# Kernel optimization log

Hardware: AMD Instinct MI355X
Metric: run time of the kernel (lower is better)

The kernel has to match this reference:

```python
import jax, jax.numpy as jnp
import numpy as np

EPS = 1e-5

def _layernorm(x, gamma, beta):
    mu = jnp.mean(x, axis=-1, keepdims=True)
    var = jnp.mean(jnp.square(x - mu), axis=-1, keepdims=True)
    return (x - mu) * jax.lax.rsqrt(var + EPS) * gamma + beta

def setup_inputs() -> dict:
    key = jax.random.key(0)
    k_in, k_w, k_b = jax.random.split(key, 3)
    d_model, d_proj, n_tok = 1024, 256, 65536
    inputs = jax.random.normal(k_in, (n_tok, d_model), dtype=jnp.float32)
    # LayerNorm(d_model) params (torch default init: gamma=1, beta=0)
    ln1_g = jnp.ones((d_model,), jnp.float32)
    ln1_b = jnp.zeros((d_model,), jnp.float32)
    # Linear(d_model, d_proj): torch stores weight as [d_proj, d_model]
    bound = 1.0 / np.sqrt(d_model)
    W = jax.random.uniform(k_w, (d_proj, d_model), jnp.float32, -bound, bound)
    b = jax.random.uniform(k_b, (d_proj,), jnp.float32, -bound, bound)
    ln2_g = jnp.ones((d_proj,), jnp.float32)
    ln2_b = jnp.zeros((d_proj,), jnp.float32)
    return {"inputs": inputs, "ln1_g": ln1_g, "ln1_b": ln1_b, "W": W, "b": b,
            "ln2_g": ln2_g, "ln2_b": ln2_b}

def reference(inputs, ln1_g, ln1_b, W, b, ln2_g, ln2_b):
    h = _layernorm(inputs, ln1_g, ln1_b)          # [N, d_model]
    h = jnp.einsum('nd,pd->np', h, W) + b          # [N, d_proj]
    return _layernorm(h, ln2_g, ln2_b)             # [N, d_proj]
```

## Files before the change

kernel.cpp:

```cpp
#include <hip/hip_runtime.h>
#include <stdint.h>


#define D_MODEL 1024
#define D_PROJ  256
#define BM      64
#define BK      32
#define KITERS  32
#define NTHR    512
#define XSTR    40
#define EPS     1e-5f

typedef __attribute__((ext_vector_type(4))) float  f32x4;
typedef __attribute__((ext_vector_type(8))) __bf16 bf16x8;

__device__ __forceinline__ void gll16(const void* g, void* l) {
  __builtin_amdgcn_global_load_lds(
      (const __attribute__((address_space(1))) uint32_t*)g,
      (__attribute__((address_space(3))) uint32_t*)l, 16, 0, 0);
}

__global__ __launch_bounds__(256) void prep_kernel(
    const float* __restrict__ W, const float* __restrict__ g1,
    const float* __restrict__ b1, const float* __restrict__ bias,
    __bf16* __restrict__ wh, __bf16* __restrict__ wl,
    float* __restrict__ s1, float* __restrict__ s2) {
  const int p = blockIdx.x;
  const int t = threadIdx.x;
  f32x4 w4  = *(const f32x4*)(W  + (size_t)p * D_MODEL + t * 4);
  f32x4 g4  = *(const f32x4*)(g1 + t * 4);
  f32x4 b14 = *(const f32x4*)(b1 + t * 4);
  union { __bf16 h[4]; uint64_t u; } ph, pl;
  float a = 0.f, c = 0.f;
#pragma unroll
  for (int j = 0; j < 4; ++j) {
    float wg = w4[j] * g4[j];
    a += wg;
    c += b14[j] * w4[j];
    __bf16 hb = (__bf16)wg;
    ph.h[j] = hb;
    pl.h[j] = (__bf16)(wg - (float)hb);
  }
  const int cc = t >> 3, g = (t >> 1) & 3, e0 = (t & 1) * 4;
  const int swz = g ^ ((p >> 1) & 3);
  *(uint64_t*)(wh + (size_t)cc * 8192 + p * 32 + swz * 8 + e0) = ph.u;
  *(uint64_t*)(wl + (size_t)p * D_MODEL + t * 4) = pl.u;
#pragma unroll
  for (int m = 1; m < 64; m <<= 1) {
    a += __shfl_xor(a, m, 64);
    c += __shfl_xor(c, m, 64);
  }
  __shared__ float ra[4], rc[4];
  if ((t & 63) == 0) { ra[t >> 6] = a; rc[t >> 6] = c; }
  __syncthreads();
  if (t == 0) {
    s1[p] = ra[0] + ra[1] + ra[2] + ra[3];
    s2[p] = rc[0] + rc[1] + rc[2] + rc[3] + bias[p];
  }
}

struct __align__(16) LdsT {
  __bf16 w[2][D_PROJ * BK];
  __bf16 xh[BM * XSTR];
  __bf16 xl[BM * XSTR];
  float  mu[BM], rs[BM];
  float  red_s[4][BM], red_q[4][BM];
};

__global__ __launch_bounds__(NTHR, 4) void fused_kernel(
    const float* __restrict__ X, const __bf16* __restrict__ wh,
    const __bf16* __restrict__ wl, const float* __restrict__ s1,
    const float* __restrict__ s2, const float* __restrict__ g2,
    const float* __restrict__ b2, float* __restrict__ out) {
  __shared__ LdsT lds;
  const int tid  = threadIdx.x;
  const int lane = tid & 63;
  const int wid  = tid >> 6;
  const int row0 = blockIdx.x * BM;
  const int lrow = lane & 15, lgrp = lane >> 4;
  const int wr = wid >> 2, wc = wid & 3;
  const int srow = tid >> 3;
  const int sc4  = (tid & 7) * 4;
  const float* xbase = X + (size_t)(row0 + srow) * D_MODEL + sc4;

#pragma unroll
  for (int call = 0; call < 2; ++call) {
    const int o = wid * 2048 + call * 1024 + lane * 16;
    gll16((const char*)wh + o, (char*)&lds.w[0][0] + wid * 2048 + call * 1024);
  }
  bf16x8 wlf0[4], wlf1[4];
#pragma unroll
  for (int n = 0; n < 4; ++n)
    wlf0[n] = *(const bf16x8*)(wl + (size_t)(wc * 64 + n * 16 + lrow) * D_MODEL + lgrp * 8);
  f32x4 xr = *(const f32x4*)xbase;

  f32x4 acc[2][4];
#pragma unroll
  for (int m = 0; m < 2; ++m)
#pragma unroll
    for (int n = 0; n < 4; ++n) acc[m][n] = (f32x4){0.f, 0.f, 0.f, 0.f};
  float ps = 0.f, pq = 0.f;

#define STEP(IT, P, WLF_CUR, WLF_NXT)                                              \
  {                                                                                \
        \
    union { __bf16 h[4]; uint64_t u; } ph_, pl_;                                   \
    _Pragma("unroll")                                                              \
    for (int j = 0; j < 4; ++j) {                                                  \
      float x = xr[j];                                                             \
      ps += x; pq += x * x;                                                        \
      __bf16 hb = (__bf16)x;                                                       \
      ph_.h[j] = hb;                                                               \
      pl_.h[j] = (__bf16)(x - (float)hb);                                          \
    }                                                                              \
    *(uint64_t*)&lds.xh[srow * XSTR + sc4] = ph_.u;                                \
    *(uint64_t*)&lds.xl[srow * XSTR + sc4] = pl_.u;                                \
       \
    __syncthreads();                                                               \
               \
    if ((IT) + 1 < KITERS) {                                                       \
      _Pragma("unroll")                                                            \
      for (int call = 0; call < 2; ++call) {                                       \
        const int o = wid * 2048 + call * 1024 + lane * 16;                        \
        gll16((const char*)wh + (((size_t)(IT) + 1) << 14) + o,                    \
              (char*)&lds.w[(P) ^ 1][0] + wid * 2048 + call * 1024);               \
      }                                                                            \
      _Pragma("unroll")                                                            \
      for (int n = 0; n < 4; ++n)                                                  \
        WLF_NXT[n] = *(const bf16x8*)(wl +                                         \
            (size_t)(wc * 64 + n * 16 + lrow) * D_MODEL + ((IT) + 1) * BK + lgrp * 8); \
      xr = *(const f32x4*)(xbase + ((IT) + 1) * BK);                               \
    }                                                                              \
                                             \
    bf16x8 ah0 = *(const bf16x8*)&lds.xh[(wr * 32 +  0 + lrow) * XSTR + lgrp * 8]; \
    bf16x8 ah1 = *(const bf16x8*)&lds.xh[(wr * 32 + 16 + lrow) * XSTR + lgrp * 8]; \
    bf16x8 al0 = *(const bf16x8*)&lds.xl[(wr * 32 +  0 + lrow) * XSTR + lgrp * 8]; \
    bf16x8 al1 = *(const bf16x8*)&lds.xl[(wr * 32 + 16 + lrow) * XSTR + lgrp * 8]; \
    _Pragma("unroll")                                                              \
    for (int n = 0; n < 4; ++n) {                                                  \
      const int pp = wc * 64 + n * 16 + lrow;                                      \
      bf16x8 bh = *(const bf16x8*)&lds.w[P][pp * 32 + (lgrp ^ ((pp >> 1) & 3)) * 8]; \
      acc[0][n] = __builtin_amdgcn_mfma_f32_16x16x32_bf16(ah0, bh, acc[0][n], 0, 0, 0); \
      acc[1][n] = __builtin_amdgcn_mfma_f32_16x16x32_bf16(ah1, bh, acc[1][n], 0, 0, 0); \
      acc[0][n] = __builtin_amdgcn_mfma_f32_16x16x32_bf16(al0, bh, acc[0][n], 0, 0, 0); \
      acc[1][n] = __builtin_amdgcn_mfma_f32_16x16x32_bf16(al1, bh, acc[1][n], 0, 0, 0); \
      acc[0][n] = __builtin_amdgcn_mfma_f32_16x16x32_bf16(ah0, WLF_CUR[n], acc[0][n], 0, 0, 0); \
      acc[1][n] = __builtin_amdgcn_mfma_f32_16x16x32_bf16(ah1, WLF_CUR[n], acc[1][n], 0, 0, 0); \
    }                                                                              \
      \
    __builtin_amdgcn_sched_barrier(0);                                             \
    __builtin_amdgcn_s_barrier();                                                  \
    __builtin_amdgcn_sched_barrier(0);                                             \
  }

  for (int it = 0; it < KITERS; it += 2) {
    STEP(it,     0, wlf0, wlf1);
    STEP(it + 1, 1, wlf1, wlf0);
  }
#undef STEP

#pragma unroll
  for (int m = 1; m < 8; m <<= 1) {
    ps += __shfl_xor(ps, m, 64);
    pq += __shfl_xor(pq, m, 64);
  }
  if ((tid & 7) == 0) {
    float mu  = ps * (1.0f / D_MODEL);
    float var = pq * (1.0f / D_MODEL) - mu * mu;
    lds.mu[srow] = mu;
    lds.rs[srow] = rsqrtf(var + EPS);
  }
  __syncthreads();

  float s1r[4], s2r[4], g2r[4], b2r[4];
#pragma unroll
  for (int n = 0; n < 4; ++n) {
    const int p = wc * 64 + n * 16 + lrow;
    s1r[n] = s1[p]; s2r[n] = s2[p];
    g2r[n] = g2[p]; b2r[n] = b2[p];
  }
#pragma unroll
  for (int m = 0; m < 2; ++m) {
#pragma unroll
    for (int j = 0; j < 4; ++j) {
      const int r = wr * 32 + m * 16 + lgrp * 4 + j;
      float muv = lds.mu[r], rsv = lds.rs[r];
      float rs_ = 0.f, rq_ = 0.f;
#pragma unroll
      for (int n = 0; n < 4; ++n) {
        float y = rsv * (acc[m][n][j] - muv * s1r[n]) + s2r[n];
        acc[m][n][j] = y;
        rs_ += y; rq_ += y * y;
      }
#pragma unroll
      for (int msk = 1; msk < 16; msk <<= 1) {
        rs_ += __shfl_xor(rs_, msk, 64);
        rq_ += __shfl_xor(rq_, msk, 64);
      }
      if (lrow == 0) { lds.red_s[wc][r] = rs_; lds.red_q[wc][r] = rq_; }
    }
  }
  __syncthreads();
#pragma unroll
  for (int m = 0; m < 2; ++m) {
#pragma unroll
    for (int j = 0; j < 4; ++j) {
      const int r = wr * 32 + m * 16 + lgrp * 4 + j;
      float S = lds.red_s[0][r] + lds.red_s[1][r] + lds.red_s[2][r] + lds.red_s[3][r];
      float Q = lds.red_q[0][r] + lds.red_q[1][r] + lds.red_q[2][r] + lds.red_q[3][r];
      float mu2  = S * (1.0f / D_PROJ);
      float var2 = Q * (1.0f / D_PROJ) - mu2 * mu2;
      float rs2  = rsqrtf(var2 + EPS);
      float* orow = out + (size_t)(row0 + r) * D_PROJ;
#pragma unroll
      for (int n = 0; n < 4; ++n)
        orow[wc * 64 + n * 16 + lrow] = (acc[m][n][j] - mu2) * rs2 * g2r[n] + b2r[n];
    }
  }
}

extern "C" void kernel_launch(void* const* d_in, const int* in_sizes, int n_in,
                              void* d_out, int out_size, void* d_ws, size_t ws_size,
                              hipStream_t stream) {
  const float* X  = (const float*)d_in[0];
  const float* g1 = (const float*)d_in[1];
  const float* b1 = (const float*)d_in[2];
  const float* W  = (const float*)d_in[3];
  const float* bb = (const float*)d_in[4];
  const float* g2 = (const float*)d_in[5];
  const float* b2 = (const float*)d_in[6];
  float* out = (float*)d_out;
  const int n_tok = in_sizes[0] / D_MODEL;

  __bf16* wh = (__bf16*)d_ws;
  __bf16* wl = wh + (size_t)KITERS * 8192;
  float*  s1 = (float*)(wl + (size_t)D_PROJ * D_MODEL);
  float*  s2 = s1 + D_PROJ;

  prep_kernel<<<D_PROJ, 256, 0, stream>>>(W, g1, b1, bb, wh, wl, s1, s2);
  fused_kernel<<<n_tok / BM, NTHR, 0, stream>>>(X, wh, wl, s1, s2, g2, b2, out);
}
```

Before: 525.4 us.

## Drop LDS staging; load X and W fragments directly from global into registers

Removes shared-memory staging of the X split-bf16 tiles and the W-high tiles. Each wave now loads its own X rows straight from global into MFMA fragment layout and reads both W high and low fragments from global (L2) every iteration, removing the per-iteration barriers. The cost is that X rows are loaded redundantly by the 4 column waves and W is fetched from cache by every wave. Occupancy hint drops from 4 to 3 blocks per CU.

After: 698.0 us. 1.33x slower.

```diff
diff --git a/kernel.cpp b/kernel.cpp
--- a/kernel.cpp
+++ b/kernel.cpp
@@ -8,17 +8,10 @@
 #define BK      32
 #define KITERS  32
 #define NTHR    512
-#define XSTR    40
 #define EPS     1e-5f
 
 typedef __attribute__((ext_vector_type(4))) float  f32x4;
 typedef __attribute__((ext_vector_type(8))) __bf16 bf16x8;
-
-__device__ __forceinline__ void gll16(const void* g, void* l) {
-  __builtin_amdgcn_global_load_lds(
-      (const __attribute__((address_space(1))) uint32_t*)g,
-      (__attribute__((address_space(3))) uint32_t*)l, 16, 0, 0);
-}
 
 __global__ __launch_bounds__(256) void prep_kernel(
     const float* __restrict__ W, const float* __restrict__ g1,
@@ -41,9 +34,7 @@
     ph.h[j] = hb;
     pl.h[j] = (__bf16)(wg - (float)hb);
   }
-  const int cc = t >> 3, g = (t >> 1) & 3, e0 = (t & 1) * 4;
-  const int swz = g ^ ((p >> 1) & 3);
-  *(uint64_t*)(wh + (size_t)cc * 8192 + p * 32 + swz * 8 + e0) = ph.u;
+  *(uint64_t*)(wh + (size_t)p * D_MODEL + t * 4) = ph.u;
   *(uint64_t*)(wl + (size_t)p * D_MODEL + t * 4) = pl.u;
 #pragma unroll
   for (int m = 1; m < 64; m <<= 1) {
@@ -59,116 +50,91 @@
   }
 }
 
-struct __align__(16) LdsT {
-  __bf16 w[2][D_PROJ * BK];
-  __bf16 xh[BM * XSTR];
-  __bf16 xl[BM * XSTR];
-  float  mu[BM], rs[BM];
-  float  red_s[4][BM], red_q[4][BM];
-};
-
-__global__ __launch_bounds__(NTHR, 4) void fused_kernel(
+__global__ __launch_bounds__(NTHR, 3) void fused_kernel(
     const float* __restrict__ X, const __bf16* __restrict__ wh,
     const __bf16* __restrict__ wl, const float* __restrict__ s1,
     const float* __restrict__ s2, const float* __restrict__ g2,
     const float* __restrict__ b2, float* __restrict__ out) {
-  __shared__ LdsT lds;
+  __shared__ float mu_s[BM], rs_s[BM];
+  __shared__ float red_s[4][BM], red_q[4][BM];
+
   const int tid  = threadIdx.x;
   const int lane = tid & 63;
   const int wid  = tid >> 6;
-  const int row0 = blockIdx.x * BM;
   const int lrow = lane & 15, lgrp = lane >> 4;
   const int wr = wid >> 2, wc = wid & 3;
-  const int srow = tid >> 3;
-  const int sc4  = (tid & 7) * 4;
-  const float* xbase = X + (size_t)(row0 + srow) * D_MODEL + sc4;
-
-#pragma unroll
-  for (int call = 0; call < 2; ++call) {
-    const int o = wid * 2048 + call * 1024 + lane * 16;
-    gll16((const char*)wh + o, (char*)&lds.w[0][0] + wid * 2048 + call * 1024);
-  }
-  bf16x8 wlf0[4], wlf1[4];
-#pragma unroll
-  for (int n = 0; n < 4; ++n)
-    wlf0[n] = *(const bf16x8*)(wl + (size_t)(wc * 64 + n * 16 + lrow) * D_MODEL + lgrp * 8);
-  f32x4 xr = *(const f32x4*)xbase;
+  const int row0 = blockIdx.x * BM;
+
+  const float* xp0 = X + (size_t)(row0 + wr * 32 + lrow) * D_MODEL + lgrp * 8;
+  const float* xp1 = xp0 + (size_t)16 * D_MODEL;
 
   f32x4 acc[2][4];
 #pragma unroll
   for (int m = 0; m < 2; ++m)
 #pragma unroll
     for (int n = 0; n < 4; ++n) acc[m][n] = (f32x4){0.f, 0.f, 0.f, 0.f};
-  float ps = 0.f, pq = 0.f;
-
-#define STEP(IT, P, WLF_CUR, WLF_NXT)                                              \
-  {                                                                                \
-        \
-    union { __bf16 h[4]; uint64_t u; } ph_, pl_;                                   \
-    _Pragma("unroll")                                                              \
-    for (int j = 0; j < 4; ++j) {                                                  \
-      float x = xr[j];                                                             \
-      ps += x; pq += x * x;                                                        \
-      __bf16 hb = (__bf16)x;                                                       \
-      ph_.h[j] = hb;                                                               \
-      pl_.h[j] = (__bf16)(x - (float)hb);                                          \
-    }                                                                              \
-    *(uint64_t*)&lds.xh[srow * XSTR + sc4] = ph_.u;                                \
-    *(uint64_t*)&lds.xl[srow * XSTR + sc4] = pl_.u;                                \
-       \
-    __syncthreads();                                                               \
-               \
-    if ((IT) + 1 < KITERS) {                                                       \
-      _Pragma("unroll")                                                            \
-      for (int call = 0; call < 2; ++call) {                                       \
-        const int o = wid * 2048 + call * 1024 + lane * 16;                        \
-        gll16((const char*)wh + (((size_t)(IT) + 1) << 14) + o,                    \
-              (char*)&lds.w[(P) ^ 1][0] + wid * 2048 + call * 1024);               \
-      }                                                                            \
-      _Pragma("unroll")                                                            \
-      for (int n = 0; n < 4; ++n)                                                  \
-        WLF_NXT[n] = *(const bf16x8*)(wl +                                         \
-            (size_t)(wc * 64 + n * 16 + lrow) * D_MODEL + ((IT) + 1) * BK + lgrp * 8); \
-      xr = *(const f32x4*)(xbase + ((IT) + 1) * BK);                               \
-    }                                                                              \
-                                             \
-    bf16x8 ah0 = *(const bf16x8*)&lds.xh[(wr * 32 +  0 + lrow) * XSTR + lgrp * 8]; \
-    bf16x8 ah1 = *(const bf16x8*)&lds.xh[(wr * 32 + 16 + lrow) * XSTR + lgrp * 8]; \
-    bf16x8 al0 = *(const bf16x8*)&lds.xl[(wr * 32 +  0 + lrow) * XSTR + lgrp * 8]; \
-    bf16x8 al1 = *(const bf16x8*)&lds.xl[(wr * 32 + 16 + lrow) * XSTR + lgrp * 8]; \
-    _Pragma("unroll")                                                              \
-    for (int n = 0; n < 4; ++n) {                                                  \
-      const int pp = wc * 64 + n * 16 + lrow;                                      \
-      bf16x8 bh = *(const bf16x8*)&lds.w[P][pp * 32 + (lgrp ^ ((pp >> 1) & 3)) * 8]; \
+  float ps0 = 0.f, pq0 = 0.f, ps1 = 0.f, pq1 = 0.f;
+
+  f32x4 xA0a = *(const f32x4*)(xp0);
+  f32x4 xA0b = *(const f32x4*)(xp0 + 4);
+  f32x4 xA1a = *(const f32x4*)(xp1);
+  f32x4 xA1b = *(const f32x4*)(xp1 + 4);
+  f32x4 xB0a, xB0b, xB1a, xB1b;
+
+#define STEP(IT, C0a, C0b, C1a, C1b, N0a, N0b, N1a, N1b)                          \
+  {                                                                               \
+    const int itn = ((IT) + 1 < KITERS) ? (IT) + 1 : (IT);                        \
+    N0a = *(const f32x4*)(xp0 + itn * BK);                                        \
+    N0b = *(const f32x4*)(xp0 + itn * BK + 4);                                    \
+    N1a = *(const f32x4*)(xp1 + itn * BK);                                        \
+    N1b = *(const f32x4*)(xp1 + itn * BK + 4);                                    \
+                                 \
+    bf16x8 ah0, al0, ah1, al1;                                                    \
+    _Pragma("unroll")                                                             \
+    for (int j = 0; j < 4; ++j) {                                                 \
+      float x = C0a[j];  ps0 += x; pq0 += x * x;                                  \
+      __bf16 hb = (__bf16)x; ah0[j] = hb; al0[j] = (__bf16)(x - (float)hb);       \
+      float y = C0b[j];  ps0 += y; pq0 += y * y;                                  \
+      __bf16 hc = (__bf16)y; ah0[4 + j] = hc; al0[4 + j] = (__bf16)(y - (float)hc);\
+      float z = C1a[j];  ps1 += z; pq1 += z * z;                                  \
+      __bf16 hd = (__bf16)z; ah1[j] = hd; al1[j] = (__bf16)(z - (float)hd);       \
+      float w = C1b[j];  ps1 += w; pq1 += w * w;                                  \
+      __bf16 he = (__bf16)w; ah1[4 + j] = he; al1[4 + j] = (__bf16)(w - (float)he);\
+    }                                                                             \
+    _Pragma("unroll")                                                             \
+    for (int n = 0; n < 4; ++n) {                                                 \
+      const size_t wo = (size_t)(wc * 64 + n * 16 + lrow) * D_MODEL +             \
+                        lgrp * 8 + (IT) * BK;                                     \
+      bf16x8 bh = *(const bf16x8*)(wh + wo);                                      \
+      bf16x8 bl = *(const bf16x8*)(wl + wo);                                      \
       acc[0][n] = __builtin_amdgcn_mfma_f32_16x16x32_bf16(ah0, bh, acc[0][n], 0, 0, 0); \
       acc[1][n] = __builtin_amdgcn_mfma_f32_16x16x32_bf16(ah1, bh, acc[1][n], 0, 0, 0); \
       acc[0][n] = __builtin_amdgcn_mfma_f32_16x16x32_bf16(al0, bh, acc[0][n], 0, 0, 0); \
       acc[1][n] = __builtin_amdgcn_mfma_f32_16x16x32_bf16(al1, bh, acc[1][n], 0, 0, 0); \
-      acc[0][n] = __builtin_amdgcn_mfma_f32_16x16x32_bf16(ah0, WLF_CUR[n], acc[0][n], 0, 0, 0); \
-      acc[1][n] = __builtin_amdgcn_mfma_f32_16x16x32_bf16(ah1, WLF_CUR[n], acc[1][n], 0, 0, 0); \
-    }                                                                              \
-      \
-    __builtin_amdgcn_sched_barrier(0);                                             \
-    __builtin_amdgcn_s_barrier();                                                  \
-    __builtin_amdgcn_sched_barrier(0);                                             \
+      acc[0][n] = __builtin_amdgcn_mfma_f32_16x16x32_bf16(ah0, bl, acc[0][n], 0, 0, 0); \
+      acc[1][n] = __builtin_amdgcn_mfma_f32_16x16x32_bf16(ah1, bl, acc[1][n], 0, 0, 0); \
+    }                                                                             \
   }
 
   for (int it = 0; it < KITERS; it += 2) {
-    STEP(it,     0, wlf0, wlf1);
-    STEP(it + 1, 1, wlf1, wlf0);
+    STEP(it,     xA0a, xA0b, xA1a, xA1b, xB0a, xB0b, xB1a, xB1b);
+    STEP(it + 1, xB0a, xB0b, xB1a, xB1b, xA0a, xA0b, xA1a, xA1b);
   }
 #undef STEP
 
-#pragma unroll
-  for (int m = 1; m < 8; m <<= 1) {
-    ps += __shfl_xor(ps, m, 64);
-    pq += __shfl_xor(pq, m, 64);
-  }
-  if ((tid & 7) == 0) {
-    float mu  = ps * (1.0f / D_MODEL);
-    float var = pq * (1.0f / D_MODEL) - mu * mu;
-    lds.mu[srow] = mu;
-    lds.rs[srow] = rsqrtf(var + EPS);
+  ps0 += __shfl_xor(ps0, 16, 64); ps0 += __shfl_xor(ps0, 32, 64);
+  pq0 += __shfl_xor(pq0, 16, 64); pq0 += __shfl_xor(pq0, 32, 64);
+  ps1 += __shfl_xor(ps1, 16, 64); ps1 += __shfl_xor(ps1, 32, 64);
+  pq1 += __shfl_xor(pq1, 16, 64); pq1 += __shfl_xor(pq1, 32, 64);
+  if (wc == 0 && lgrp == 0) {
+    float mu0 = ps0 * (1.0f / D_MODEL);
+    float v0  = pq0 * (1.0f / D_MODEL) - mu0 * mu0;
+    mu_s[wr * 32 + lrow] = mu0;
+    rs_s[wr * 32 + lrow] = rsqrtf(v0 + EPS);
+    float mu1 = ps1 * (1.0f / D_MODEL);
+    float v1  = pq1 * (1.0f / D_MODEL) - mu1 * mu1;
+    mu_s[wr * 32 + 16 + lrow] = mu1;
+    rs_s[wr * 32 + 16 + lrow] = rsqrtf(v1 + EPS);
   }
   __syncthreads();
 
@@ -184,7 +150,7 @@
 #pragma unroll
     for (int j = 0; j < 4; ++j) {
       const int r = wr * 32 + m * 16 + lgrp * 4 + j;
-      float muv = lds.mu[r], rsv = lds.rs[r];
+      float muv = mu_s[r], rsv = rs_s[r];
       float rs_ = 0.f, rq_ = 0.f;
 #pragma unroll
       for (int n = 0; n < 4; ++n) {
@@ -197,7 +163,7 @@
         rs_ += __shfl_xor(rs_, msk, 64);
         rq_ += __shfl_xor(rq_, msk, 64);
       }
-      if (lrow == 0) { lds.red_s[wc][r] = rs_; lds.red_q[wc][r] = rq_; }
+      if (lrow == 0) { red_s[wc][r] = rs_; red_q[wc][r] = rq_; }
     }
   }
   __syncthreads();
@@ -206,8 +172,8 @@
 #pragma unroll
     for (int j = 0; j < 4; ++j) {
       const int r = wr * 32 + m * 16 + lgrp * 4 + j;
-      float S = lds.red_s[0][r] + lds.red_s[1][r] + lds.red_s[2][r] + lds.red_s[3][r];
-      float Q = lds.red_q[0][r] + lds.red_q[1][r] + lds.red_q[2][r] + lds.red_q[3][r];
+      float S = red_s[0][r] + red_s[1][r] + red_s[2][r] + red_s[3][r];
+      float Q = red_q[0][r] + red_q[1][r] + red_q[2][r] + red_q[3][r];
       float mu2  = S * (1.0f / D_PROJ);
       float var2 = Q * (1.0f / D_PROJ) - mu2 * mu2;
       float rs2  = rsqrtf(var2 + EPS);
@@ -233,7 +199,7 @@
   const int n_tok = in_sizes[0] / D_MODEL;
 
   __bf16* wh = (__bf16*)d_ws;
-  __bf16* wl = wh + (size_t)KITERS * 8192;
+  __bf16* wl = wh + (size_t)D_PROJ * D_MODEL;
   float*  s1 = (float*)(wl + (size_t)D_PROJ * D_MODEL);
   float*  s2 = s1 + D_PROJ;
 
```
